# Performance work log

Measured on AMD Instinct MI355X. Metric: run time of the kernel, lower is better.

Reference implementation:

```python
import jax, jax.numpy as jnp
import numpy as np

EPS = 1e-5


def gcn_conv(x, src, dst, n_nodes, W, b):
    # x: [B, N, Fin]; src/dst: [E+N] (self loops included); W: [Fout, Fin]
    h = jnp.einsum('bnf,of->bno', x, W)                      # [B, N, Fout]
    deg = jnp.zeros((n_nodes,), h.dtype).at[dst].add(1.0)    # in-degree of A+I
    dinv = jnp.where(deg > 0, 1.0 / jnp.sqrt(deg), 0.0)
    norm = dinv[src] * dinv[dst]                             # [E+N]
    msg = h[:, src, :] * norm[None, :, None]                 # gather along node axis
    out = jnp.zeros_like(h).at[:, dst, :].add(msg)           # scatter-add aggregate
    return out + b


def batchnorm_nodes(x, gamma, beta):
    # torch BatchNorm1d(N) on [B, N, C]: channel axis is N, stats over (B, C)
    mean = jnp.mean(x, axis=(0, 2), keepdims=True)
    var = jnp.mean(jnp.square(x - mean), axis=(0, 2), keepdims=True)
    xn = (x - mean) * jax.lax.rsqrt(var + EPS)
    return xn * gamma[None, :, None] + beta[None, :, None]


def setup_inputs() -> dict:
    key = jax.random.key(0)
    ks = jax.random.split(key, 20)
    B, N, FIN, D, OUT, E = 4096, 64, 67, 2048, 2, 512
    s = 0.1
    d = {}
    d['x_fingerprints'] = jax.random.normal(ks[0], (B, D), jnp.float32)
    d['x_node_features'] = jax.random.normal(ks[1], (B, N, FIN), jnp.float32)
    d['edge_list'] = jax.random.randint(ks[2], (2, E), 0, N)
    d['W1'] = jax.random.normal(ks[3], (64, FIN), jnp.float32) * s
    d['b1'] = jax.random.normal(ks[4], (64,), jnp.float32) * s
    d['g1'] = 1.0 + jax.random.normal(ks[5], (N,), jnp.float32) * s
    d['be1'] = jax.random.normal(ks[6], (N,), jnp.float32) * s
    d['W2'] = jax.random.normal(ks[7], (32, 64), jnp.float32) * s
    d['b2'] = jax.random.normal(ks[8], (32,), jnp.float32) * s
    d['g2'] = 1.0 + jax.random.normal(ks[9], (N,), jnp.float32) * s
    d['be2'] = jax.random.normal(ks[10], (N,), jnp.float32) * s
    d['Wl1'] = jax.random.normal(ks[11], (400, D), jnp.float32) * (s / 4)
    d['bl1'] = jax.random.normal(ks[12], (400,), jnp.float32) * s
    d['Wl2'] = jax.random.normal(ks[13], (64, 400), jnp.float32) * s
    d['bl2'] = jax.random.normal(ks[14], (64,), jnp.float32) * s
    d['Wfc'] = jax.random.normal(ks[15], (OUT, 96), jnp.float32) * s
    d['bfc'] = jax.random.normal(ks[16], (OUT,), jnp.float32) * s
    return d


def reference(x_fingerprints, x_node_features, edge_list, W1, b1, g1, be1,
              W2, b2, g2, be2, Wl1, bl1, Wl2, bl2, Wfc, bfc):
    B, N, _ = x_node_features.shape
    loops = jnp.arange(N)
    src = jnp.concatenate([edge_list[0], loops])  # add self loops (GCNConv default)
    dst = jnp.concatenate([edge_list[1], loops])
    g = gcn_conv(x_node_features, src, dst, N, W1, b1)
    g = jax.nn.relu(batchnorm_nodes(g, g1, be1))
    g = gcn_conv(g, src, dst, N, W2, b2)
    g = jax.nn.relu(batchnorm_nodes(g, g2, be2))           # [B, N, 32]
    pooled = jnp.max(g, axis=1)                             # global_max_pool -> [B, 32]
    h = jax.nn.relu(x_fingerprints @ Wl1.T + bl1)
    h = jax.nn.relu(h @ Wl2.T + bl2)                        # [B, 64]
    out = jnp.concatenate([pooled, h], axis=1) @ Wfc.T + bfc
    return out
```

## Files before the change

### kernel.cpp

```cpp
#include <hip/hip_runtime.h>
#include <hip/hip_bf16.h>
#include <math.h>

typedef __bf16 bf16;
typedef __attribute__((ext_vector_type(8))) __bf16 bf16x8;
typedef __attribute__((ext_vector_type(4))) __bf16 bf16x4;
typedef __attribute__((ext_vector_type(4))) float f32x4;

#define EPSBN 1e-5f
#define B_    4096
#define N_    64
#define FIN_  67
#define E_    512
#define NSLOT 128

__global__ __launch_bounds__(256) void k0_prep(const int* __restrict__ edge,
    const float* __restrict__ W1, const float* __restrict__ W2,
    float* __restrict__ partials,
    bf16* __restrict__ an_hi, bf16* __restrict__ an_lo,
    bf16* __restrict__ wpad,
    bf16* __restrict__ w2pad)
{
    int tid = threadIdx.x;
    for (int i = blockIdx.x * 256 + tid; i < NSLOT * 64 * 4; i += gridDim.x * 256)
        partials[i] = 0.f;
    if (blockIdx.x == 1) {
        for (int i = tid; i < 64 * 104; i += 256) {
            int n = i / 104, f = i % 104;
            wpad[i] = (f < FIN_) ? (bf16)W1[n * FIN_ + f] : (bf16)0.f;
        }
        return;
    }
    if (blockIdx.x == 2) {
        for (int i = tid; i < 32 * 72; i += 256) {
            int o = i / 72, f = i % 72;
            w2pad[i] = (f < 64) ? (bf16)W2[o * 64 + f] : (bf16)0.f;
        }
        return;
    }
    if (blockIdx.x != 0) return;

    __shared__ float An[64 * 64];
    __shared__ int ssrc[E_], sdst[E_];
    __shared__ int deg[N_];
    __shared__ float dinv[N_];
    for (int i = tid; i < 64 * 64; i += 256) An[i] = 0.f;
    for (int i = tid; i < E_; i += 256) { ssrc[i] = edge[i]; sdst[i] = edge[E_ + i]; }
    if (tid < N_) deg[tid] = 1;
    __syncthreads();
    for (int i = tid; i < E_; i += 256) atomicAdd(&deg[sdst[i]], 1);
    __syncthreads();
    if (tid < N_) dinv[tid] = rsqrtf((float)deg[tid]);
    __syncthreads();
    for (int i = tid; i < E_; i += 256) {
        int s = ssrc[i], d = sdst[i];
        atomicAdd(&An[d * 64 + s], dinv[s] * dinv[d]);
    }
    if (tid < N_) atomicAdd(&An[tid * 64 + tid], dinv[tid] * dinv[tid]);
    __syncthreads();
    for (int i = tid; i < 64 * 64; i += 256) {
        float v = An[i];
        bf16 h = (bf16)v;
        an_hi[i] = h;
        an_lo[i] = (bf16)(v - (float)h);
    }
}

__global__ __launch_bounds__(256, 3) void k1_gcn1(
    const float* __restrict__ x,
    const float* __restrict__ b1,
    const bf16* __restrict__ an_hi, const bf16* __restrict__ an_lo,
    const bf16* __restrict__ wpad,
    bf16* __restrict__ g1out,
    float* __restrict__ part1)
{
    __shared__ float xraw[4352];
    __shared__ bf16 hhi[64 * 72];
    __shared__ bf16 hlo[64 * 72];
    __shared__ bf16 ost[64 * 72];

    int tid = threadIdx.x;
    int w = tid >> 6, lane = tid & 63, q = lane >> 4, r15 = lane & 15;
    int arow = w * 16 + r15;

    bf16x8 wf[3][4];
#pragma unroll
    for (int kt = 0; kt < 3; ++kt)
#pragma unroll
        for (int nt = 0; nt < 4; ++nt)
            wf[kt][nt] = *(const bf16x8*)&wpad[(nt * 16 + r15) * 104 + kt * 32 + q * 8];

    const bf16* ahp = an_hi + arow * 64 + q * 8;
    const bf16* alp = an_lo + arow * 64 + q * 8;
    bf16x8 Ah0 = *(const bf16x8*)ahp;
    bf16x8 Ah1 = *(const bf16x8*)(ahp + 32);
    bf16x8 Al0 = *(const bf16x8*)alp;
    bf16x8 Al1 = *(const bf16x8*)(alp + 32);

    float bc[4];
#pragma unroll
    for (int nt = 0; nt < 4; ++nt) bc[nt] = b1[nt * 16 + r15];

    size_t b0 = (size_t)blockIdx.x * 4;
    const f32x4* xb4 = (const f32x4*)(x + b0 * 4288);

    f32x4 pre0 = xb4[tid], pre1 = xb4[tid + 256], pre2 = xb4[tid + 512], pre3 = xb4[tid + 768];
    f32x4 pre4 = {0.f, 0.f, 0.f, 0.f};
    if (tid < 48) pre4 = xb4[tid + 1024];

    f32x4* xl4 = (f32x4*)xraw;
    f32x4 z4 = {0.f, 0.f, 0.f, 0.f};

#pragma unroll 1
    for (int g = 0; g < 4; ++g) {
        int b = (int)b0 + g;
        xl4[tid] = pre0; xl4[tid + 256] = pre1; xl4[tid + 512] = pre2; xl4[tid + 768] = pre3;
        if (tid < 48) xl4[tid + 1024] = pre4;
        __syncthreads();

        f32x4 acc[4] = {z4, z4, z4, z4};
        const float* xr = xraw + arow * FIN_;
#pragma unroll
        for (int kt = 0; kt < 3; ++kt) {
            bf16x8 a;
            if (kt < 2) {
                int k0 = kt * 32 + q * 8;
#pragma unroll
                for (int j = 0; j < 8; ++j) a[j] = (bf16)xr[k0 + j];
            } else {
#pragma unroll
                for (int j = 0; j < 8; ++j) a[j] = (bf16)0.f;
                if (q == 0) { a[0] = (bf16)xr[64]; a[1] = (bf16)xr[65]; a[2] = (bf16)xr[66]; }
            }
#pragma unroll
            for (int nt = 0; nt < 4; ++nt)
                acc[nt] = __builtin_amdgcn_mfma_f32_16x16x32_bf16(a, wf[kt][nt], acc[nt], 0, 0, 0);
        }
        if (g < 3) {
            const f32x4* xn = xb4 + (size_t)(g + 1) * 1072;
            pre0 = xn[tid]; pre1 = xn[tid + 256]; pre2 = xn[tid + 512]; pre3 = xn[tid + 768];
            if (tid < 48) pre4 = xn[tid + 1024];
        }
        __syncthreads();

        int sbase = w * 16 + q * 4;
#pragma unroll
        for (int nt = 0; nt < 4; ++nt) {
            int c = nt * 16 + r15;
            bf16x4 hi, lo;
#pragma unroll
            for (int r = 0; r < 4; ++r) {
                float v = acc[nt][r];
                bf16 h = (bf16)v;
                hi[r] = h; lo[r] = (bf16)(v - (float)h);
            }
            *(bf16x4*)&hhi[c * 72 + sbase] = hi;
            *(bf16x4*)&hlo[c * 72 + sbase] = lo;
        }
        __syncthreads();

        f32x4 acc2[4] = {z4, z4, z4, z4};
#pragma unroll
        for (int kt = 0; kt < 2; ++kt) {
            bf16x8 Ahk = kt ? Ah1 : Ah0;
            bf16x8 Alk = kt ? Al1 : Al0;
#pragma unroll
            for (int nt = 0; nt < 4; ++nt) {
                int o = (nt * 16 + r15) * 72 + kt * 32 + q * 8;
                bf16x8 Hh = *(const bf16x8*)&hhi[o];
                bf16x8 Hl = *(const bf16x8*)&hlo[o];
                acc2[nt] = __builtin_amdgcn_mfma_f32_16x16x32_bf16(Ahk, Hh, acc2[nt], 0, 0, 0);
                acc2[nt] = __builtin_amdgcn_mfma_f32_16x16x32_bf16(Ahk, Hl, acc2[nt], 0, 0, 0);
                acc2[nt] = __builtin_amdgcn_mfma_f32_16x16x32_bf16(Alk, Hh, acc2[nt], 0, 0, 0);
            }
        }
#pragma unroll
        for (int nt = 0; nt < 4; ++nt) {
            int c = nt * 16 + r15;
#pragma unroll
            for (int r = 0; r < 4; ++r)
                ost[(sbase + r) * 72 + c] = (bf16)(acc2[nt][r] + bc[nt]);
        }
        __syncthreads();

        int n = tid >> 2, oq = tid & 3;
        bf16x8 o0 = *(const bf16x8*)&ost[n * 72 + oq * 16];
        bf16x8 o1 = *(const bf16x8*)&ost[n * 72 + oq * 16 + 8];
        bf16* gp = g1out + ((size_t)b * 4096 + n * 64 + oq * 16);
        *(bf16x8*)gp = o0;
        *(bf16x8*)(gp + 8) = o1;
        float s1 = 0.f, s2 = 0.f;
#pragma unroll
        for (int j = 0; j < 8; ++j) {
            float v0 = (float)o0[j], v1 = (float)o1[j];
            s1 += v0 + v1; s2 += v0 * v0 + v1 * v1;
        }
        s1 += __shfl_xor(s1, 1); s1 += __shfl_xor(s1, 2);
        s2 += __shfl_xor(s2, 1); s2 += __shfl_xor(s2, 2);
        if (oq == 0) {
            int slot = b & (NSLOT - 1);
            atomicAdd(&part1[(slot * 64 + n) * 2 + 0], s1);
            atomicAdd(&part1[(slot * 64 + n) * 2 + 1], s2);
        }
    }
}

__global__ __launch_bounds__(64) void k_bnstats(
    const float* __restrict__ part,
    const float* __restrict__ gamma, const float* __restrict__ beta,
    float* __restrict__ scale, float* __restrict__ shift, float inv_count)
{
    int n = blockIdx.x, t = threadIdx.x;
    float s1 = part[(t * 64 + n) * 2] + part[((t + 64) * 64 + n) * 2];
    float s2 = part[(t * 64 + n) * 2 + 1] + part[((t + 64) * 64 + n) * 2 + 1];
#pragma unroll
    for (int o = 32; o > 0; o >>= 1) { s1 += __shfl_down(s1, o); s2 += __shfl_down(s2, o); }
    if (t == 0) {
        float mean = s1 * inv_count;
        float var = s2 * inv_count - mean * mean;
        float sc = gamma[n] * rsqrtf(var + EPSBN);
        scale[n] = sc;
        shift[n] = beta[n] - mean * sc;
    }
}

__global__ __launch_bounds__(256, 4) void k3_gcn2(
    const bf16* __restrict__ g1out,
    const float* __restrict__ b2,
    const float* __restrict__ scale1, const float* __restrict__ shift1,
    const bf16* __restrict__ an_hi, const bf16* __restrict__ an_lo,
    const bf16* __restrict__ w2pad,
    bf16* __restrict__ g2out,
    float* __restrict__ part2)
{
    __shared__ bf16 ya[64 * 72];
    __shared__ bf16 hhi[32 * 72];
    __shared__ bf16 hlo[32 * 72];
    __shared__ bf16 ost[64 * 40];

    int tid = threadIdx.x;
    int w = tid >> 6, lane = tid & 63, q = lane >> 4, r15 = lane & 15;
    int arow = w * 16 + r15;

    bf16x8 wf[2][2];
#pragma unroll
    for (int kt = 0; kt < 2; ++kt)
#pragma unroll
        for (int nt = 0; nt < 2; ++nt)
            wf[kt][nt] = *(const bf16x8*)&w2pad[(nt * 16 + r15) * 72 + kt * 32 + q * 8];

    const bf16* ahp = an_hi + arow * 64 + q * 8;
    const bf16* alp = an_lo + arow * 64 + q * 8;
    bf16x8 Ah0 = *(const bf16x8*)ahp;
    bf16x8 Ah1 = *(const bf16x8*)(ahp + 32);
    bf16x8 Al0 = *(const bf16x8*)alp;
    bf16x8 Al1 = *(const bf16x8*)(alp + 32);
    float sc = scale1[arow], sh = shift1[arow];
    float bc[2] = { b2[r15], b2[16 + r15] };

    size_t b0 = (size_t)blockIdx.x * 4;
    const bf16x8* gg8 = (const bf16x8*)(g1out + b0 * 4096);
    bf16x8 p0 = gg8[tid], p1 = gg8[tid + 256];

    int r0 = tid >> 3, c0 = (tid & 7) * 8;
    f32x4 z4 = {0.f, 0.f, 0.f, 0.f};

#pragma unroll 1
    for (int g = 0; g < 4; ++g) {
        int b = (int)b0 + g;
        *(bf16x8*)&ya[r0 * 72 + c0] = p0;
        *(bf16x8*)&ya[(r0 + 32) * 72 + c0] = p1;
        __syncthreads();

        f32x4 acc[2] = {z4, z4};
#pragma unroll
        for (int kt = 0; kt < 2; ++kt) {
            int k0 = kt * 32 + q * 8;
            bf16x8 raw = *(const bf16x8*)&ya[arow * 72 + k0];
            bf16x8 a;
#pragma unroll
            for (int j = 0; j < 8; ++j)
                a[j] = (bf16)fmaxf(fmaf(sc, (float)raw[j], sh), 0.f);
#pragma unroll
            for (int nt = 0; nt < 2; ++nt)
                acc[nt] = __builtin_amdgcn_mfma_f32_16x16x32_bf16(a, wf[kt][nt], acc[nt], 0, 0, 0);
        }
        if (g < 3) {
            p0 = gg8[(size_t)(g + 1) * 512 + tid];
            p1 = gg8[(size_t)(g + 1) * 512 + tid + 256];
        }
        __syncthreads();

        int sbase = w * 16 + q * 4;
#pragma unroll
        for (int nt = 0; nt < 2; ++nt) {
            int c = nt * 16 + r15;
            bf16x4 hi, lo;
#pragma unroll
            for (int r = 0; r < 4; ++r) {
                float v = acc[nt][r];
                bf16 h = (bf16)v;
                hi[r] = h; lo[r] = (bf16)(v - (float)h);
            }
            *(bf16x4*)&hhi[c * 72 + sbase] = hi;
            *(bf16x4*)&hlo[c * 72 + sbase] = lo;
        }
        __syncthreads();

        f32x4 acc2[2] = {z4, z4};
#pragma unroll
        for (int kt = 0; kt < 2; ++kt) {
            bf16x8 Ahk = kt ? Ah1 : Ah0;
            bf16x8 Alk = kt ? Al1 : Al0;
#pragma unroll
            for (int nt = 0; nt < 2; ++nt) {
                int o = (nt * 16 + r15) * 72 + kt * 32 + q * 8;
                bf16x8 Hh = *(const bf16x8*)&hhi[o];
                bf16x8 Hl = *(const bf16x8*)&hlo[o];
                acc2[nt] = __builtin_amdgcn_mfma_f32_16x16x32_bf16(Ahk, Hh, acc2[nt], 0, 0, 0);
                acc2[nt] = __builtin_amdgcn_mfma_f32_16x16x32_bf16(Ahk, Hl, acc2[nt], 0, 0, 0);
                acc2[nt] = __builtin_amdgcn_mfma_f32_16x16x32_bf16(Alk, Hh, acc2[nt], 0, 0, 0);
            }
        }
#pragma unroll
        for (int nt = 0; nt < 2; ++nt) {
            int c = nt * 16 + r15;
#pragma unroll
            for (int r = 0; r < 4; ++r)
                ost[(sbase + r) * 40 + c] = (bf16)(acc2[nt][r] + bc[nt]);
        }
        __syncthreads();

        int n = tid >> 2, oq = tid & 3;
        bf16x8 ov = *(const bf16x8*)&ost[n * 40 + oq * 8];
        *(bf16x8*)(g2out + ((size_t)b * 2048 + n * 32 + oq * 8)) = ov;
        float s1 = 0.f, s2 = 0.f;
#pragma unroll
        for (int j = 0; j < 8; ++j) {
            float v = (float)ov[j];
            s1 += v; s2 += v * v;
        }
        s1 += __shfl_xor(s1, 1); s1 += __shfl_xor(s1, 2);
        s2 += __shfl_xor(s2, 1); s2 += __shfl_xor(s2, 2);
        if (oq == 0) {
            int slot = b & (NSLOT - 1);
            atomicAdd(&part2[(slot * 64 + n) * 2 + 0], s1);
            atomicAdd(&part2[(slot * 64 + n) * 2 + 1], s2);
        }
    }
}

__global__ __launch_bounds__(256) void k6_mlp1(
    const float* __restrict__ A,
    const float* __restrict__ Bw,
    float* __restrict__ part)
{
    __shared__ bf16 As[64 * 36];
    __shared__ bf16 Bs[64 * 36];
    int tid = threadIdx.x;
    int m0 = blockIdx.x * 64, n0 = blockIdx.y * 64, ks = blockIdx.z;
    int row = tid >> 2, seg = tid & 3;
    int w = tid >> 6, lane = tid & 63, q = lane >> 4, r15 = lane & 15;
    f32x4 z4 = {0.f, 0.f, 0.f, 0.f};
    f32x4 acc[4] = {z4, z4, z4, z4};
    const float* pA = A + (size_t)(m0 + row) * 2048 + ks * 512 + seg * 8;
    bool bvalid = (n0 + row) < 400;
    const float* pB = Bw + (size_t)(n0 + row) * 2048 + ks * 512 + seg * 8;

    f32x4 a0 = *(const f32x4*)pA;
    f32x4 a1 = *(const f32x4*)(pA + 4);
    f32x4 c0 = z4, c1 = z4;
    if (bvalid) { c0 = *(const f32x4*)pB; c1 = *(const f32x4*)(pB + 4); }

    for (int kt = 0; kt < 16; ++kt) {
        bf16x8 apk, bpk;
        apk[0] = (bf16)a0[0]; apk[1] = (bf16)a0[1]; apk[2] = (bf16)a0[2]; apk[3] = (bf16)a0[3];
        apk[4] = (bf16)a1[0]; apk[5] = (bf16)a1[1]; apk[6] = (bf16)a1[2]; apk[7] = (bf16)a1[3];
        bpk[0] = (bf16)c0[0]; bpk[1] = (bf16)c0[1]; bpk[2] = (bf16)c0[2]; bpk[3] = (bf16)c0[3];
        bpk[4] = (bf16)c1[0]; bpk[5] = (bf16)c1[1]; bpk[6] = (bf16)c1[2]; bpk[7] = (bf16)c1[3];
        __syncthreads();
        *(bf16x8*)&As[row * 36 + seg * 8] = apk;
        *(bf16x8*)&Bs[row * 36 + seg * 8] = bpk;
        __syncthreads();
        if (kt < 15) {
            pA += 32; pB += 32;
            a0 = *(const f32x4*)pA; a1 = *(const f32x4*)(pA + 4);
            if (bvalid) { c0 = *(const f32x4*)pB; c1 = *(const f32x4*)(pB + 4); }
        }
        bf16x8 a = *(const bf16x8*)&As[(w * 16 + r15) * 36 + q * 8];
#pragma unroll
        for (int nt = 0; nt < 4; ++nt) {
            bf16x8 bb = *(const bf16x8*)&Bs[(nt * 16 + r15) * 36 + q * 8];
            acc[nt] = __builtin_amdgcn_mfma_f32_16x16x32_bf16(a, bb, acc[nt], 0, 0, 0);
        }
    }
    float* pp = part + (size_t)ks * 1638400;
#pragma unroll
    for (int nt = 0; nt < 4; ++nt)
#pragma unroll
        for (int r = 0; r < 4; ++r) {
            int mm = m0 + w * 16 + q * 4 + r;
            int nn = n0 + nt * 16 + r15;
            if (nn < 400) pp[(size_t)mm * 400 + nn] = acc[nt][r];
        }
}

__global__ __launch_bounds__(256) void k6_reduce(
    const float* __restrict__ part,
    const float* __restrict__ bias,
    bf16* __restrict__ h1)
{
    int i = blockIdx.x * 256 + threadIdx.x;
    const f32x4* p = (const f32x4*)part;
    f32x4 s0 = p[i], s1v = p[i + 409600], s2v = p[i + 819200], s3v = p[i + 1228800];
    int nn = (i * 4) % 400;
    f32x4 bv = *(const f32x4*)&bias[nn];
    bf16x4 ov;
    ov[0] = (bf16)fmaxf(s0[0] + s1v[0] + s2v[0] + s3v[0] + bv[0], 0.f);
    ov[1] = (bf16)fmaxf(s0[1] + s1v[1] + s2v[1] + s3v[1] + bv[1], 0.f);
    ov[2] = (bf16)fmaxf(s0[2] + s1v[2] + s2v[2] + s3v[2] + bv[2], 0.f);
    ov[3] = (bf16)fmaxf(s0[3] + s1v[3] + s2v[3] + s3v[3] + bv[3], 0.f);
    *(bf16x4*)&h1[i * 4] = ov;
}

__global__ __launch_bounds__(256) void k7_mlp2(
    const bf16* __restrict__ A,
    const float* __restrict__ Bw,
    const float* __restrict__ bias,
    float* __restrict__ Cout)
{
    __shared__ bf16 As[16 * 416];
    int tid = threadIdx.x;
    int m0 = blockIdx.x * 16;
    for (int i = tid; i < 16 * 50; i += 256) {
        int rr = i / 50, cc = (i % 50) * 8;
        *(bf16x8*)&As[rr * 416 + cc] = *(const bf16x8*)(A + (size_t)(m0 + rr) * 400 + cc);
    }
    if (tid < 32) {
        int rr = tid >> 1, cc = 400 + (tid & 1) * 8;
        bf16x8 z;
#pragma unroll
        for (int k = 0; k < 8; ++k) z[k] = (bf16)0.f;
        *(bf16x8*)&As[rr * 416 + cc] = z;
    }
    __syncthreads();

    int w = tid >> 6, lane = tid & 63, q = lane >> 4, r15 = lane & 15;
    f32x4 acc = {0.f, 0.f, 0.f, 0.f};
    const float* pB = Bw + (size_t)(w * 16 + r15) * 400;
#pragma unroll 4
    for (int kt = 0; kt < 13; ++kt) {
        int k0 = kt * 32 + q * 8;
        bf16x8 a = *(const bf16x8*)&As[r15 * 416 + k0];
        bf16x8 bb;
#pragma unroll
        for (int k = 0; k < 8; ++k) bb[k] = (bf16)0.f;
        if (k0 < 400) {
            f32x4 c0 = *(const f32x4*)(pB + k0);
            f32x4 c1 = *(const f32x4*)(pB + k0 + 4);
            bb[0] = (bf16)c0[0]; bb[1] = (bf16)c0[1]; bb[2] = (bf16)c0[2]; bb[3] = (bf16)c0[3];
            bb[4] = (bf16)c1[0]; bb[5] = (bf16)c1[1]; bb[6] = (bf16)c1[2]; bb[7] = (bf16)c1[3];
        }
        acc = __builtin_amdgcn_mfma_f32_16x16x32_bf16(a, bb, acc, 0, 0, 0);
    }
#pragma unroll
    for (int r = 0; r < 4; ++r) {
        int mm = m0 + q * 4 + r;
        int nn = w * 16 + r15;
        float v = fmaxf(acc[r] + bias[nn], 0.f);
        Cout[(size_t)mm * 64 + nn] = v;
    }
}

__global__ __launch_bounds__(256) void k8_final(
    const bf16* __restrict__ g2out,
    const float* __restrict__ scale2, const float* __restrict__ shift2,
    const float* __restrict__ h2,
    const float* __restrict__ Wfc,
    const float* __restrict__ bfc,
    float* __restrict__ out)
{
    __shared__ float s2s[64], sh2s[64];
    int tid = threadIdx.x;
    if (tid < 64) { s2s[tid] = scale2[tid]; sh2s[tid] = shift2[tid]; }
    __syncthreads();
    int w = tid >> 6, lane = tid & 63;
    int b = blockIdx.x * 4 + w;
    int c = lane & 31, half = lane >> 5;
    const bf16* gb = g2out + (size_t)b * 2048;
    float mx = 0.f;
    for (int i = 0; i < 32; ++i) {
        int n = half * 32 + i;
        float v = (float)gb[n * 32 + c];
        float val = fmaf(s2s[n], v, sh2s[n]);
        mx = fmaxf(mx, val);
    }
    mx = fmaxf(mx, __shfl_xor(mx, 32));
    float h2v = h2[(size_t)b * 64 + lane];
#pragma unroll
    for (int o = 0; o < 2; ++o) {
        float t = h2v * Wfc[o * 96 + 32 + lane];
        if (half == 0) t += mx * Wfc[o * 96 + c];
#pragma unroll
        for (int off = 32; off > 0; off >>= 1) t += __shfl_xor(t, off);
        if (lane == 0) out[(size_t)b * 2 + o] = t + bfc[o];
    }
}

extern "C" void kernel_launch(void* const* d_in, const int* in_sizes, int n_in,
                              void* d_out, int out_size, void* d_ws, size_t ws_size,
                              hipStream_t stream)
{
    const float* x_fp   = (const float*)d_in[0];
    const float* x_node = (const float*)d_in[1];
    const int*   edge   = (const int*)d_in[2];
    const float* W1     = (const float*)d_in[3];
    const float* b1     = (const float*)d_in[4];
    const float* g1     = (const float*)d_in[5];
    const float* be1    = (const float*)d_in[6];
    const float* W2     = (const float*)d_in[7];
    const float* b2     = (const float*)d_in[8];
    const float* g2     = (const float*)d_in[9];
    const float* be2    = (const float*)d_in[10];
    const float* Wl1    = (const float*)d_in[11];
    const float* bl1    = (const float*)d_in[12];
    const float* Wl2    = (const float*)d_in[13];
    const float* bl2    = (const float*)d_in[14];
    const float* Wfc    = (const float*)d_in[15];
    const float* bfc    = (const float*)d_in[16];
    float* out = (float*)d_out;

    char* ws = (char*)d_ws;
    float* scale1  = (float*)(ws + 5632);
    float* shift1  = (float*)(ws + 5888);
    float* scale2  = (float*)(ws + 6144);
    float* shift2  = (float*)(ws + 6400);
    float* part1   = (float*)(ws + 8192);
    float* part2   = (float*)(ws + 8192 + 65536);
    bf16*  g1out   = (bf16*)(ws + 139264);
    float* part6   = (float*)(ws + 139264);
    bf16*  g2out   = (bf16*)(ws + 33693696ull);
    bf16*  h1      = (bf16*)(ws + 50470912ull);
    float* h2      = (float*)(ws + 53747712ull);
    bf16*  an_hi   = (bf16*)(ws + 53747712ull);
    bf16*  an_lo   = (bf16*)(ws + 53747712ull + 8192);
    bf16*  wpad    = (bf16*)(ws + 53747712ull + 16384);
    bf16*  w2pad   = (bf16*)(ws + 53747712ull + 32768);

    k0_prep<<<dim3(64), dim3(256), 0, stream>>>(edge, W1, W2, part1, an_hi, an_lo, wpad, w2pad);
    k1_gcn1<<<dim3(1024), dim3(256), 0, stream>>>(x_node, b1, an_hi, an_lo, wpad, g1out, part1);
    k_bnstats<<<dim3(64), dim3(64), 0, stream>>>(part1, g1, be1, scale1, shift1,
                                                 1.f / (4096.f * 64.f));
    k3_gcn2<<<dim3(1024), dim3(256), 0, stream>>>(g1out, b2, scale1, shift1,
                                                  an_hi, an_lo, w2pad, g2out, part2);
    k_bnstats<<<dim3(64), dim3(64), 0, stream>>>(part2, g2, be2, scale2, shift2,
                                                 1.f / (4096.f * 32.f));
    k6_mlp1<<<dim3(64, 7, 4), dim3(256), 0, stream>>>(x_fp, Wl1, part6);
    k6_reduce<<<dim3(1600), dim3(256), 0, stream>>>(part6, bl1, h1);
    k7_mlp2<<<dim3(256), dim3(256), 0, stream>>>(h1, Wl2, bl2, h2);
    k8_final<<<dim3(1024), dim3(256), 0, stream>>>(g2out, scale2, shift2, h2, Wfc, bfc, out);
}
```

Baseline: 241.3 us.

## Fuse split-K reduce into MLP2, double-buffer MLP1 B tiles, alias GCN1 smem

Three changes. The split-K partial-sum reduction, bias and ReLU for the first MLP layer now run inside the second MLP kernel's A-tile load, which removes one launch and the round trip of the bf16 h1 buffer. The first MLP kernel now loads A fragments straight into registers instead of staging them in shared memory, and double-buffers B tiles of 64 K per step, cutting barriers from two per 32-K step to one per 64-K step, with a hint of 4 blocks per SM. GCN1 overlays its x staging buffer with its hi/lo buffers in a union to shrink LDS use, which may raise occupancy.

```diff
diff --git a/kernel.cpp b/kernel.cpp
--- a/kernel.cpp
+++ b/kernel.cpp
@@ -13,6 +13,13 @@
 #define FIN_  67
 #define E_    512
 #define NSLOT 128
+
+__device__ inline bf16x8 pack8(f32x4 lo, f32x4 hi) {
+    bf16x8 r;
+    r[0] = (bf16)lo[0]; r[1] = (bf16)lo[1]; r[2] = (bf16)lo[2]; r[3] = (bf16)lo[3];
+    r[4] = (bf16)hi[0]; r[5] = (bf16)hi[1]; r[6] = (bf16)hi[2]; r[7] = (bf16)hi[3];
+    return r;
+}
 
 __global__ __launch_bounds__(256) void k0_prep(const int* __restrict__ edge,
     const float* __restrict__ W1, const float* __restrict__ W2,
@@ -74,9 +81,10 @@
     bf16* __restrict__ g1out,
     float* __restrict__ part1)
 {
-    __shared__ float xraw[4352];
-    __shared__ bf16 hhi[64 * 72];
-    __shared__ bf16 hlo[64 * 72];
+    __shared__ union {
+        float xraw[4352];
+        struct { bf16 hhi[64 * 72]; bf16 hlo[64 * 72]; } h;
+    } u;
     __shared__ bf16 ost[64 * 72];
 
     int tid = threadIdx.x;
@@ -108,7 +116,7 @@
     f32x4 pre4 = {0.f, 0.f, 0.f, 0.f};
     if (tid < 48) pre4 = xb4[tid + 1024];
 
-    f32x4* xl4 = (f32x4*)xraw;
+    f32x4* xl4 = (f32x4*)u.xraw;
     f32x4 z4 = {0.f, 0.f, 0.f, 0.f};
 
 #pragma unroll 1
@@ -119,7 +127,7 @@
         __syncthreads();
 
         f32x4 acc[4] = {z4, z4, z4, z4};
-        const float* xr = xraw + arow * FIN_;
+        const float* xr = u.xraw + arow * FIN_;
 #pragma unroll
         for (int kt = 0; kt < 3; ++kt) {
             bf16x8 a;
@@ -154,8 +162,8 @@
                 bf16 h = (bf16)v;
                 hi[r] = h; lo[r] = (bf16)(v - (float)h);
             }
-            *(bf16x4*)&hhi[c * 72 + sbase] = hi;
-            *(bf16x4*)&hlo[c * 72 + sbase] = lo;
+            *(bf16x4*)&u.h.hhi[c * 72 + sbase] = hi;
+            *(bf16x4*)&u.h.hlo[c * 72 + sbase] = lo;
         }
         __syncthreads();
 
@@ -167,8 +175,8 @@
 #pragma unroll
             for (int nt = 0; nt < 4; ++nt) {
                 int o = (nt * 16 + r15) * 72 + kt * 32 + q * 8;
-                bf16x8 Hh = *(const bf16x8*)&hhi[o];
-                bf16x8 Hl = *(const bf16x8*)&hlo[o];
+                bf16x8 Hh = *(const bf16x8*)&u.h.hhi[o];
+                bf16x8 Hl = *(const bf16x8*)&u.h.hlo[o];
                 acc2[nt] = __builtin_amdgcn_mfma_f32_16x16x32_bf16(Ahk, Hh, acc2[nt], 0, 0, 0);
                 acc2[nt] = __builtin_amdgcn_mfma_f32_16x16x32_bf16(Ahk, Hl, acc2[nt], 0, 0, 0);
                 acc2[nt] = __builtin_amdgcn_mfma_f32_16x16x32_bf16(Alk, Hh, acc2[nt], 0, 0, 0);
@@ -350,48 +358,65 @@
     }
 }
 
-__global__ __launch_bounds__(256) void k6_mlp1(
+__global__ __launch_bounds__(256, 4) void k6_mlp1(
     const float* __restrict__ A,
     const float* __restrict__ Bw,
     float* __restrict__ part)
 {
-    __shared__ bf16 As[64 * 36];
-    __shared__ bf16 Bs[64 * 36];
+    __shared__ bf16 Bs[2][64 * 72];
     int tid = threadIdx.x;
     int m0 = blockIdx.x * 64, n0 = blockIdx.y * 64, ks = blockIdx.z;
-    int row = tid >> 2, seg = tid & 3;
     int w = tid >> 6, lane = tid & 63, q = lane >> 4, r15 = lane & 15;
+    int brow = tid >> 2, bs8 = (tid & 3) * 16;
+    bool bvalid = (n0 + brow) < 400;
+    const float* pA = A + (size_t)(m0 + w * 16 + r15) * 2048 + ks * 512 + q * 8;
+    const float* pB = Bw + (size_t)(n0 + brow) * 2048 + ks * 512 + bs8;
     f32x4 z4 = {0.f, 0.f, 0.f, 0.f};
     f32x4 acc[4] = {z4, z4, z4, z4};
-    const float* pA = A + (size_t)(m0 + row) * 2048 + ks * 512 + seg * 8;
-    bool bvalid = (n0 + row) < 400;
-    const float* pB = Bw + (size_t)(n0 + row) * 2048 + ks * 512 + seg * 8;
-
-    f32x4 a0 = *(const f32x4*)pA;
-    f32x4 a1 = *(const f32x4*)(pA + 4);
-    f32x4 c0 = z4, c1 = z4;
-    if (bvalid) { c0 = *(const f32x4*)pB; c1 = *(const f32x4*)(pB + 4); }
-
-    for (int kt = 0; kt < 16; ++kt) {
-        bf16x8 apk, bpk;
-        apk[0] = (bf16)a0[0]; apk[1] = (bf16)a0[1]; apk[2] = (bf16)a0[2]; apk[3] = (bf16)a0[3];
-        apk[4] = (bf16)a1[0]; apk[5] = (bf16)a1[1]; apk[6] = (bf16)a1[2]; apk[7] = (bf16)a1[3];
-        bpk[0] = (bf16)c0[0]; bpk[1] = (bf16)c0[1]; bpk[2] = (bf16)c0[2]; bpk[3] = (bf16)c0[3];
-        bpk[4] = (bf16)c1[0]; bpk[5] = (bf16)c1[1]; bpk[6] = (bf16)c1[2]; bpk[7] = (bf16)c1[3];
-        __syncthreads();
-        *(bf16x8*)&As[row * 36 + seg * 8] = apk;
-        *(bf16x8*)&Bs[row * 36 + seg * 8] = bpk;
-        __syncthreads();
-        if (kt < 15) {
-            pA += 32; pB += 32;
-            a0 = *(const f32x4*)pA; a1 = *(const f32x4*)(pA + 4);
-            if (bvalid) { c0 = *(const f32x4*)pB; c1 = *(const f32x4*)(pB + 4); }
-        }
-        bf16x8 a = *(const bf16x8*)&As[(w * 16 + r15) * 36 + q * 8];
+
+    f32x4 a0 = *(const f32x4*)pA,        a1 = *(const f32x4*)(pA + 4);
+    f32x4 a2 = *(const f32x4*)(pA + 32), a3 = *(const f32x4*)(pA + 36);
+    f32x4 b0 = z4, b1 = z4, b2 = z4, b3 = z4;
+    if (bvalid) {
+        b0 = *(const f32x4*)pB;       b1 = *(const f32x4*)(pB + 4);
+        b2 = *(const f32x4*)(pB + 8); b3 = *(const f32x4*)(pB + 12);
+    }
+    *(bf16x8*)&Bs[0][brow * 72 + bs8]     = pack8(b0, b1);
+    *(bf16x8*)&Bs[0][brow * 72 + bs8 + 8] = pack8(b2, b3);
+    __syncthreads();
+
+#pragma unroll
+    for (int t = 0; t < 8; ++t) {
+        f32x4 na0, na1, na2, na3;
+        f32x4 nb0 = z4, nb1 = z4, nb2 = z4, nb3 = z4;
+        if (t < 7) {
+            const float* qA = pA + (t + 1) * 64;
+            na0 = *(const f32x4*)qA;        na1 = *(const f32x4*)(qA + 4);
+            na2 = *(const f32x4*)(qA + 32); na3 = *(const f32x4*)(qA + 36);
+            if (bvalid) {
+                const float* qB = pB + (t + 1) * 64;
+                nb0 = *(const f32x4*)qB;       nb1 = *(const f32x4*)(qB + 4);
+                nb2 = *(const f32x4*)(qB + 8); nb3 = *(const f32x4*)(qB + 12);
+            }
+        }
+        bf16x8 af0 = pack8(a0, a1), af1 = pack8(a2, a3);
+        const bf16* cur = Bs[t & 1];
 #pragma unroll
         for (int nt = 0; nt < 4; ++nt) {
-            bf16x8 bb = *(const bf16x8*)&Bs[(nt * 16 + r15) * 36 + q * 8];
-            acc[nt] = __builtin_amdgcn_mfma_f32_16x16x32_bf16(a, bb, acc[nt], 0, 0, 0);
+            bf16x8 bb = *(const bf16x8*)&cur[(nt * 16 + r15) * 72 + q * 8];
+            acc[nt] = __builtin_amdgcn_mfma_f32_16x16x32_bf16(af0, bb, acc[nt], 0, 0, 0);
+        }
+#pragma unroll
+        for (int nt = 0; nt < 4; ++nt) {
+            bf16x8 bb = *(const bf16x8*)&cur[(nt * 16 + r15) * 72 + 32 + q * 8];
+            acc[nt] = __builtin_amdgcn_mfma_f32_16x16x32_bf16(af1, bb, acc[nt], 0, 0, 0);
+        }
+        if (t < 7) {
+            bf16* nxt = (bf16*)Bs[(t & 1) ^ 1];
+            *(bf16x8*)&nxt[brow * 72 + bs8]     = pack8(nb0, nb1);
+            *(bf16x8*)&nxt[brow * 72 + bs8 + 8] = pack8(nb2, nb3);
+            __syncthreads();
+            a0 = na0; a1 = na1; a2 = na2; a3 = na3;
         }
     }
     float* pp = part + (size_t)ks * 1638400;
@@ -405,26 +430,9 @@
         }
 }
 
-__global__ __launch_bounds__(256) void k6_reduce(
+__global__ __launch_bounds__(256) void k7_mlp2(
     const float* __restrict__ part,
-    const float* __restrict__ bias,
-    bf16* __restrict__ h1)
-{
-    int i = blockIdx.x * 256 + threadIdx.x;
-    const f32x4* p = (const f32x4*)part;
-    f32x4 s0 = p[i], s1v = p[i + 409600], s2v = p[i + 819200], s3v = p[i + 1228800];
-    int nn = (i * 4) % 400;
-    f32x4 bv = *(const f32x4*)&bias[nn];
-    bf16x4 ov;
-    ov[0] = (bf16)fmaxf(s0[0] + s1v[0] + s2v[0] + s3v[0] + bv[0], 0.f);
-    ov[1] = (bf16)fmaxf(s0[1] + s1v[1] + s2v[1] + s3v[1] + bv[1], 0.f);
-    ov[2] = (bf16)fmaxf(s0[2] + s1v[2] + s2v[2] + s3v[2] + bv[2], 0.f);
-    ov[3] = (bf16)fmaxf(s0[3] + s1v[3] + s2v[3] + s3v[3] + bv[3], 0.f);
-    *(bf16x4*)&h1[i * 4] = ov;
-}
-
-__global__ __launch_bounds__(256) void k7_mlp2(
-    const bf16* __restrict__ A,
+    const float* __restrict__ bl1,
     const float* __restrict__ Bw,
     const float* __restrict__ bias,
     float* __restrict__ Cout)
@@ -432,9 +440,21 @@
     __shared__ bf16 As[16 * 416];
     int tid = threadIdx.x;
     int m0 = blockIdx.x * 16;
-    for (int i = tid; i < 16 * 50; i += 256) {
+    for (int i = tid; i < 800; i += 256) {
         int rr = i / 50, cc = (i % 50) * 8;
-        *(bf16x8*)&As[rr * 416 + cc] = *(const bf16x8*)(A + (size_t)(m0 + rr) * 400 + cc);
+        const float* p0 = part + (size_t)(m0 + rr) * 400 + cc;
+        f32x4 x0 = *(const f32x4*)p0,             x1 = *(const f32x4*)(p0 + 4);
+        f32x4 y0 = *(const f32x4*)(p0 + 1638400), y1 = *(const f32x4*)(p0 + 1638404);
+        f32x4 u0 = *(const f32x4*)(p0 + 3276800), u1 = *(const f32x4*)(p0 + 3276804);
+        f32x4 v0 = *(const f32x4*)(p0 + 4915200), v1 = *(const f32x4*)(p0 + 4915204);
+        f32x4 w0 = *(const f32x4*)&bl1[cc],       w1 = *(const f32x4*)&bl1[cc + 4];
+        bf16x8 o;
+#pragma unroll
+        for (int j = 0; j < 4; ++j) {
+            o[j]     = (bf16)fmaxf(x0[j] + y0[j] + u0[j] + v0[j] + w0[j], 0.f);
+            o[4 + j] = (bf16)fmaxf(x1[j] + y1[j] + u1[j] + v1[j] + w1[j], 0.f);
+        }
+        *(bf16x8*)&As[rr * 416 + cc] = o;
     }
     if (tid < 32) {
         int rr = tid >> 1, cc = 400 + (tid & 1) * 8;
@@ -540,7 +560,6 @@
     bf16*  g1out   = (bf16*)(ws + 139264);
     float* part6   = (float*)(ws + 139264);
     bf16*  g2out   = (bf16*)(ws + 33693696ull);
-    bf16*  h1      = (bf16*)(ws + 50470912ull);
     float* h2      = (float*)(ws + 53747712ull);
     bf16*  an_hi   = (bf16*)(ws + 53747712ull);
     bf16*  an_lo   = (bf16*)(ws + 53747712ull + 8192);
@@ -556,7 +575,6 @@
     k_bnstats<<<dim3(64), dim3(64), 0, stream>>>(part2, g2, be2, scale2, shift2,
                                                  1.f / (4096.f * 32.f));
     k6_mlp1<<<dim3(64, 7, 4), dim3(256), 0, stream>>>(x_fp, Wl1, part6);
-    k6_reduce<<<dim3(1600), dim3(256), 0, stream>>>(part6, bl1, h1);
-    k7_mlp2<<<dim3(256), dim3(256), 0, stream>>>(h1, Wl2, bl2, h2);
+    k7_mlp2<<<dim3(256), dim3(256), 0, stream>>>(part6, bl1, Wl2, bl2, h2);
     k8_final<<<dim3(1024), dim3(256), 0, stream>>>(g2out, scale2, shift2, h2, Wfc, bfc, out);
 }
```

New measurement: 247.3 us. 1.02x slower.
